# Performance work log

Measured on AMD Instinct MI355X. Metric: run time of the kernel, lower is better.

The kernel has to match this reference:

```python
import jax, jax.numpy as jnp
import numpy as np

B = 32
L = 256
NUM_AA = 20
LAMBDA_SINGLE = 1.0
LAMBDA_PAIR = 0.2 * (L - 1)


def setup_inputs() -> dict:
    key = jax.random.key(0)
    k1, k2, k3 = jax.random.split(key, 3)
    x = jax.random.randint(k1, (B, L), 0, NUM_AA, dtype=jnp.int32)
    # Embedding(num, 1) init: normal(0, embedding_dim**-0.5) = std 1.0
    w_single = jax.random.normal(k2, (L * NUM_AA, 1), dtype=jnp.float32)
    w_pair = jax.random.normal(k3, (L * L * NUM_AA * NUM_AA, 1), dtype=jnp.float32)
    return {"x": x, "w_single": w_single, "w_pair": w_pair}


def reference(x, w_single, w_pair):
    ws = w_single[:, 0]  # [L*20]
    wp = w_pair[:, 0]    # [L*L*400]
    Bn, Ln = x.shape
    pos = jnp.arange(Ln, dtype=jnp.int32)

    # singles[b, i] = ws[i*20 + x[b, i]]
    singles = ws[pos[None, :] * NUM_AA + x]  # [B, L]
    all_singles = jnp.broadcast_to(ws.reshape(Ln, NUM_AA), (Bn, Ln, NUM_AA))  # [B, L, 20]

    # pairs[b, i, j] = wp[(i*L + j)*400 + x[b,i]*20 + x[b,j]]
    idx_pairs = (pos[:, None] * Ln + pos[None, :]) * (NUM_AA * NUM_AA) \
        + x[:, :, None] * NUM_AA + x[:, None, :]  # [B, L, L]
    pairs = wp[idx_pairs]  # [B, L, L]

    # all_pairs reproduces the original in-place mutation semantics:
    # at outer iteration i (inner loop over j), x[:, p] has already been
    # overwritten to 19 for p < i, equals j for p == i, and is original for p > i.
    i_ax = pos[None, :, None, None]                      # [1, L, 1, 1]
    p_ax = pos[None, None, :, None]                      # [1, 1, L, 1]
    j_ax = jnp.arange(NUM_AA, dtype=jnp.int32)[None, None, None, :]  # [1,1,1,20]
    x_b = x[:, None, :, None]                            # [B, 1, L, 1]
    eff = jnp.where(p_ax < i_ax, NUM_AA - 1, jnp.where(p_ax == i_ax, j_ax, x_b))
    idx_all = (i_ax * Ln + p_ax) * (NUM_AA * NUM_AA) + j_ax * NUM_AA + eff  # [B,L,L,20]
    all_pairs = wp[idx_all]  # [B, L, L, 20]

    energy = singles + jnp.sum(pairs, axis=2)  # [B, L]
    logits = all_singles + jnp.sum(all_pairs, axis=2)  # [B, L, 20]
    total_energy = jax.nn.logsumexp(logits, axis=-1)  # [B, L]
    final_energy = jnp.mean(jnp.sum(-energy + total_energy, axis=1))

    single_reg = LAMBDA_SINGLE * jnp.sum(jnp.square(w_single))
    pair_reg = LAMBDA_PAIR * jnp.sum(jnp.square(w_pair))
    single_lasso = LAMBDA_SINGLE * jnp.sum(jnp.abs(w_single))
    pair_lasso = LAMBDA_PAIR * jnp.sum(jnp.abs(w_pair))
    return final_energy + single_reg + pair_reg + single_lasso + pair_lasso
```

## Files before the change

### kernel.cpp

```cpp
#include <hip/hip_runtime.h>
#include <cmath>

#define Bsz 32
#define Lsz 256
#define Asz 20
#define NCHUNK 8
#define PCH 32
#define GRP 16
#define NGRP 2
#define BLK1 640

#define OFF_G 0
#define OFF_C (NCHUNK*Lsz*Bsz*Asz)
#define OFF_E (OFF_C + NCHUNK*Lsz*Asz)
#define OFF_RSQ (OFF_E + NCHUNK*Lsz*Bsz)
#define OFF_RAB (OFF_RSQ + NCHUNK*Lsz)
#define OFF_K2  (OFF_RAB + NCHUNK*Lsz)

__global__ __launch_bounds__(BLK1, 8) void k1(const int* __restrict__ x,
                                              const float* __restrict__ wp,
                                              float* __restrict__ ws) {
  const int wg = blockIdx.x;
  const int c = wg & (NCHUNK - 1);
  const int i = wg >> 3;
  const int t = threadIdx.x;
  const int j = t >> 5;
  const int b = t & 31;

  __shared__ float blk[GRP * 400];
  __shared__ int   xs[PCH * Bsz];
  __shared__ int   xi[Bsz];
  __shared__ float wred[32];

  const int pbase = c * PCH;
  for (int k = t; k < PCH * Bsz; k += BLK1) {
    int dp = k >> 5, bb = k & 31;
    xs[k] = x[bb * Lsz + pbase + dp];
  }
  if (t < Bsz) xi[t] = x[t * Lsz + i];

  float accJ = 0.f, accE = 0.f, accC = 0.f, rsq = 0.f, rab = 0.f;

  const float4* wrow = (const float4*)(wp + (size_t)(i * Lsz + pbase) * 400);
  float4 v0 = wrow[t];
  float4 v1 = wrow[t + 640];
  float4 v2 = (t < 320) ? wrow[t + 1280] : make_float4(0.f, 0.f, 0.f, 0.f);

  for (int g = 0; g < NGRP; ++g) {
    float4* bf4 = (float4*)blk;
    bf4[t] = v0;
    bf4[t + 640] = v1;
    if (t < 320) bf4[t + 1280] = v2;
    rsq += v0.x*v0.x + v0.y*v0.y + v0.z*v0.z + v0.w*v0.w;
    rsq += v1.x*v1.x + v1.y*v1.y + v1.z*v1.z + v1.w*v1.w;
    rab += fabsf(v0.x)+fabsf(v0.y)+fabsf(v0.z)+fabsf(v0.w);
    rab += fabsf(v1.x)+fabsf(v1.y)+fabsf(v1.z)+fabsf(v1.w);
    if (t < 320) {
      rsq += v2.x*v2.x + v2.y*v2.y + v2.z*v2.z + v2.w*v2.w;
      rab += fabsf(v2.x)+fabsf(v2.y)+fabsf(v2.z)+fabsf(v2.w);
    }
    __syncthreads();

    if (g == 0) {
      v0 = wrow[1600 + t];
      v1 = wrow[1600 + t + 640];
      if (t < 320) v2 = wrow[1600 + t + 1280];
    }

    const int p0 = pbase + g * GRP;
    int ppstart = i + 1 - p0;
    if (ppstart < 0) ppstart = 0;
    const int jbase = j * Asz;
    for (int pp = ppstart; pp < GRP; ++pp) {
      int xv = xs[((g * GRP + pp) << 5) | b];
      accJ += blk[pp * 400 + jbase + xv];
    }
    if (t < Bsz) {
      const int ebase = xi[t] * Asz;
      for (int pp = 0; pp < GRP; ++pp) {
        int xv = xs[((g * GRP + pp) << 5) | t];
        accE += blk[pp * 400 + ebase + xv];
      }
    } else if (t < Bsz + Asz) {
      const int jj = t - Bsz;
      int pend = i - p0;
      if (pend > GRP) pend = GRP;
      for (int pp = 0; pp < pend; ++pp) accC += blk[pp * 400 + jj * Asz + 19];
      const int pd = i - p0;
      if (pd >= 0 && pd < GRP) accC += blk[pd * 400 + jj * Asz + jj];
    }
    __syncthreads();
  }

  ws[OFF_G + ((size_t)(c * Lsz + i) * Bsz + b) * Asz + j] = accJ;
  if (t < Bsz) ws[OFF_E + (c * Lsz + i) * Bsz + t] = accE;
  else if (t < Bsz + Asz) ws[OFF_C + (c * Lsz + i) * Asz + (t - Bsz)] = accC;

  for (int s = 32; s >= 1; s >>= 1) {
    rsq += __shfl_down(rsq, s);
    rab += __shfl_down(rab, s);
  }
  if ((t & 63) == 0) { wred[t >> 6] = rsq; wred[16 + (t >> 6)] = rab; }
  __syncthreads();
  if (t == 0) {
    float a = 0.f, bb = 0.f;
    for (int w = 0; w < 10; ++w) { a += wred[w]; bb += wred[16 + w]; }
    ws[OFF_RSQ + wg] = a;
    ws[OFF_RAB + wg] = bb;
  }
}

__global__ __launch_bounds__(BLK1) void k2(const int* __restrict__ x,
                                           const float* __restrict__ wsng,
                                           const float* __restrict__ ws,
                                           float* __restrict__ wso) {
  const int i = blockIdx.x;
  const int t = threadIdx.x;
  const int j = t >> 5, b = t & 31;
  __shared__ float l[Bsz * 21];

  float v = wsng[i * Asz + j];
  #pragma unroll
  for (int c = 0; c < NCHUNK; ++c) {
    v += ws[OFF_C + (c * Lsz + i) * Asz + j];
    v += ws[OFF_G + ((size_t)(c * Lsz + i) * Bsz + b) * Asz + j];
  }
  l[b * 21 + j] = v;
  __syncthreads();

  if (t < Bsz) {
    float m = -1e30f;
    #pragma unroll
    for (int jj = 0; jj < Asz; ++jj) m = fmaxf(m, l[t * 21 + jj]);
    float se = 0.f;
    #pragma unroll
    for (int jj = 0; jj < Asz; ++jj) se += __expf(l[t * 21 + jj] - m);
    float lse = m + __logf(se);
    float en = wsng[i * Asz + x[t * Lsz + i]];
    #pragma unroll
    for (int c = 0; c < NCHUNK; ++c) en += ws[OFF_E + (c * Lsz + i) * Bsz + t];
    wso[OFF_K2 + i * Bsz + t] = lse - en;
  }
}

__global__ __launch_bounds__(256) void k3(const float* __restrict__ wsng,
                                          const float* __restrict__ ws,
                                          float* __restrict__ out) {
  const int t = threadIdx.x;
  float ssq = 0.f, sab = 0.f;
  for (int k = t; k < Lsz * Asz; k += 256) {
    float v = wsng[k];
    ssq += v * v; sab += fabsf(v);
  }
  float psq = 0.f, pab = 0.f;
  for (int k = t; k < NCHUNK * Lsz; k += 256) {
    psq += ws[OFF_RSQ + k];
    pab += ws[OFF_RAB + k];
  }
  float fe = 0.f;
  for (int k = t; k < Lsz * Bsz; k += 256) fe += ws[OFF_K2 + k];

  const float LP = 51.0f;
  float val = fe * (1.0f / Bsz) + (ssq + sab) + LP * (psq + pab);

  __shared__ float red[256];
  red[t] = val;
  __syncthreads();
  for (int s = 128; s >= 1; s >>= 1) {
    if (t < s) red[t] += red[t + s];
    __syncthreads();
  }
  if (t == 0) out[0] = red[0];
}

extern "C" void kernel_launch(void* const* d_in, const int* in_sizes, int n_in,
                              void* d_out, int out_size, void* d_ws, size_t ws_size,
                              hipStream_t stream) {
  const int*   x       = (const int*)d_in[0];
  const float* wsingle = (const float*)d_in[1];
  const float* wpair   = (const float*)d_in[2];
  float* ws  = (float*)d_ws;
  float* out = (float*)d_out;

  k1<<<Lsz * NCHUNK, BLK1, 0, stream>>>(x, wpair, ws);
  k2<<<Lsz, BLK1, 0, stream>>>(x, wsingle, ws, ws);
  k3<<<1, 256, 0, stream>>>(wsingle, ws, out);
}
```

Before: 178.1 us.

## Shrink k1 blocks to 256 threads with smaller groups and balanced block order

Reduces the k1 block from 640 to 256 threads, and each thread now accumulates up to three amino-acid columns. Weight rows are staged in groups of 8 positions instead of 16, which halves shared memory per block, and the register prefetch of the next group is dropped. Blocks are paired so that triangle-heavy (i, chunk) tiles sit next to light ones. The x values are stored as bytes and the partial-sum layout is transposed so that k2 reads it coalesced. In exchange the kernel gives up explicit load/compute overlap and adds an extra barrier per group.

Measured after the change: 182.9 us. +2.7%, slower.

```diff
diff --git a/kernel.cpp b/kernel.cpp
--- a/kernel.cpp
+++ b/kernel.cpp
@@ -6,9 +6,9 @@
 #define Asz 20
 #define NCHUNK 8
 #define PCH 32
-#define GRP 16
-#define NGRP 2
-#define BLK1 640
+#define GRP 8
+#define NGRP 4
+#define BLK1 256
 
 #define OFF_G 0
 #define OFF_C (NCHUNK*Lsz*Bsz*Asz)
@@ -21,99 +21,98 @@
                                               const float* __restrict__ wp,
                                               float* __restrict__ ws) {
   const int wg = blockIdx.x;
-  const int c = wg & (NCHUNK - 1);
-  const int i = wg >> 3;
+  const int u = ((wg >> 4) << 3) | (wg & 7);
+  const int h = (wg >> 3) & 1;
+  const int i = h ? (255 - (u >> 3)) : (u >> 3);
+  const int c = h ? (7 - (u & 7)) : (u & 7);
+
   const int t = threadIdx.x;
-  const int j = t >> 5;
   const int b = t & 31;
+  const int jg = t >> 5;
 
   __shared__ float blk[GRP * 400];
-  __shared__ int   xs[PCH * Bsz];
-  __shared__ int   xi[Bsz];
-  __shared__ float wred[32];
+  __shared__ unsigned char xs[PCH * Bsz];
+  __shared__ int xi[Bsz];
+  __shared__ float wred[8];
 
   const int pbase = c * PCH;
   for (int k = t; k < PCH * Bsz; k += BLK1) {
     int dp = k >> 5, bb = k & 31;
-    xs[k] = x[bb * Lsz + pbase + dp];
+    xs[k] = (unsigned char)x[bb * Lsz + pbase + dp];
   }
   if (t < Bsz) xi[t] = x[t * Lsz + i];
 
-  float accJ = 0.f, accE = 0.f, accC = 0.f, rsq = 0.f, rab = 0.f;
+  float aJ0 = 0.f, aJ1 = 0.f, aJ2 = 0.f, accE = 0.f, accC = 0.f;
+  float rsq = 0.f, rab = 0.f;
 
-  const float4* wrow = (const float4*)(wp + (size_t)(i * Lsz + pbase) * 400);
-  float4 v0 = wrow[t];
-  float4 v1 = wrow[t + 640];
-  float4 v2 = (t < 320) ? wrow[t + 1280] : make_float4(0.f, 0.f, 0.f, 0.f);
+  const float4* wrow4 = (const float4*)(wp + (size_t)(i * Lsz + pbase) * 400);
+  const int j0 = jg * 20, j1 = (jg + 8) * 20, j2 = (jg + 16) * 20;
 
   for (int g = 0; g < NGRP; ++g) {
-    float4* bf4 = (float4*)blk;
-    bf4[t] = v0;
-    bf4[t + 640] = v1;
-    if (t < 320) bf4[t + 1280] = v2;
-    rsq += v0.x*v0.x + v0.y*v0.y + v0.z*v0.z + v0.w*v0.w;
-    rsq += v1.x*v1.x + v1.y*v1.y + v1.z*v1.z + v1.w*v1.w;
-    rab += fabsf(v0.x)+fabsf(v0.y)+fabsf(v0.z)+fabsf(v0.w);
-    rab += fabsf(v1.x)+fabsf(v1.y)+fabsf(v1.z)+fabsf(v1.w);
-    if (t < 320) {
-      rsq += v2.x*v2.x + v2.y*v2.y + v2.z*v2.z + v2.w*v2.w;
-      rab += fabsf(v2.x)+fabsf(v2.y)+fabsf(v2.z)+fabsf(v2.w);
+    __syncthreads();
+    {
+      float4* bf4 = (float4*)blk;
+      const float4* src = wrow4 + g * 800;
+      for (int k = t; k < 800; k += BLK1) {
+        float4 v = src[k];
+        bf4[k] = v;
+        rsq += v.x*v.x + v.y*v.y + v.z*v.z + v.w*v.w;
+        rab += fabsf(v.x)+fabsf(v.y)+fabsf(v.z)+fabsf(v.w);
+      }
     }
     __syncthreads();
 
-    if (g == 0) {
-      v0 = wrow[1600 + t];
-      v1 = wrow[1600 + t + 640];
-      if (t < 320) v2 = wrow[1600 + t + 1280];
+    const int p0 = pbase + g * GRP;
+    int pps = i + 1 - p0; if (pps < 0) pps = 0;
+    for (int pp = pps; pp < GRP; ++pp) {
+      int xv = xs[((g * GRP + pp) << 5) | b];
+      const float* bp = blk + pp * 400 + xv;
+      aJ0 += bp[j0];
+      aJ1 += bp[j1];
+      if (jg < 4) aJ2 += bp[j2];
     }
-
-    const int p0 = pbase + g * GRP;
-    int ppstart = i + 1 - p0;
-    if (ppstart < 0) ppstart = 0;
-    const int jbase = j * Asz;
-    for (int pp = ppstart; pp < GRP; ++pp) {
-      int xv = xs[((g * GRP + pp) << 5) | b];
-      accJ += blk[pp * 400 + jbase + xv];
+    if (t >= 64 && t < 96) {
+      const int be = t - 64;
+      const int eb = xi[be] * Asz;
+      for (int pp = 0; pp < GRP; ++pp) {
+        int xv = xs[((g * GRP + pp) << 5) | be];
+        accE += blk[pp * 400 + eb + xv];
+      }
     }
-    if (t < Bsz) {
-      const int ebase = xi[t] * Asz;
-      for (int pp = 0; pp < GRP; ++pp) {
-        int xv = xs[((g * GRP + pp) << 5) | t];
-        accE += blk[pp * 400 + ebase + xv];
-      }
-    } else if (t < Bsz + Asz) {
-      const int jj = t - Bsz;
-      int pend = i - p0;
-      if (pend > GRP) pend = GRP;
+    if (t >= 128 && t < 148) {
+      const int jj = t - 128;
+      int pend = i - p0; if (pend > GRP) pend = GRP;
       for (int pp = 0; pp < pend; ++pp) accC += blk[pp * 400 + jj * Asz + 19];
       const int pd = i - p0;
-      if (pd >= 0 && pd < GRP) accC += blk[pd * 400 + jj * Asz + jj];
+      if (pd >= 0 && pd < GRP) accC += blk[pd * 400 + jj * (Asz + 1)];
     }
-    __syncthreads();
   }
 
-  ws[OFF_G + ((size_t)(c * Lsz + i) * Bsz + b) * Asz + j] = accJ;
-  if (t < Bsz) ws[OFF_E + (c * Lsz + i) * Bsz + t] = accE;
-  else if (t < Bsz + Asz) ws[OFF_C + (c * Lsz + i) * Asz + (t - Bsz)] = accC;
+  {
+    float* G = ws + OFF_G + (size_t)(c * Lsz + i) * (Bsz * Asz);
+    G[jg * 32 + b] = aJ0;
+    G[(jg + 8) * 32 + b] = aJ1;
+    if (jg < 4) G[(jg + 16) * 32 + b] = aJ2;
+  }
+  if (t >= 64 && t < 96)   ws[OFF_E + (c * Lsz + i) * Bsz + (t - 64)]  = accE;
+  if (t >= 128 && t < 148) ws[OFF_C + (c * Lsz + i) * Asz + (t - 128)] = accC;
 
   for (int s = 32; s >= 1; s >>= 1) {
     rsq += __shfl_down(rsq, s);
     rab += __shfl_down(rab, s);
   }
-  if ((t & 63) == 0) { wred[t >> 6] = rsq; wred[16 + (t >> 6)] = rab; }
+  if ((t & 63) == 0) { wred[t >> 6] = rsq; wred[4 + (t >> 6)] = rab; }
   __syncthreads();
   if (t == 0) {
-    float a = 0.f, bb = 0.f;
-    for (int w = 0; w < 10; ++w) { a += wred[w]; bb += wred[16 + w]; }
-    ws[OFF_RSQ + wg] = a;
-    ws[OFF_RAB + wg] = bb;
+    ws[OFF_RSQ + wg] = wred[0] + wred[1] + wred[2] + wred[3];
+    ws[OFF_RAB + wg] = wred[4] + wred[5] + wred[6] + wred[7];
   }
 }
 
-__global__ __launch_bounds__(BLK1) void k2(const int* __restrict__ x,
-                                           const float* __restrict__ wsng,
-                                           const float* __restrict__ ws,
-                                           float* __restrict__ wso) {
+__global__ __launch_bounds__(640) void k2(const int* __restrict__ x,
+                                          const float* __restrict__ wsng,
+                                          const float* __restrict__ ws,
+                                          float* __restrict__ wso) {
   const int i = blockIdx.x;
   const int t = threadIdx.x;
   const int j = t >> 5, b = t & 31;
@@ -123,7 +122,7 @@
   #pragma unroll
   for (int c = 0; c < NCHUNK; ++c) {
     v += ws[OFF_C + (c * Lsz + i) * Asz + j];
-    v += ws[OFF_G + ((size_t)(c * Lsz + i) * Bsz + b) * Asz + j];
+    v += ws[OFF_G + (size_t)(c * Lsz + i) * (Bsz * Asz) + t];
   }
   l[b * 21 + j] = v;
   __syncthreads();
@@ -183,6 +182,6 @@
   float* out = (float*)d_out;
 
   k1<<<Lsz * NCHUNK, BLK1, 0, stream>>>(x, wpair, ws);
-  k2<<<Lsz, BLK1, 0, stream>>>(x, wsingle, ws, ws);
+  k2<<<Lsz, 640, 0, stream>>>(x, wsingle, ws, ws);
   k3<<<1, 256, 0, stream>>>(wsingle, ws, out);
 }
```
